# Optimization experiments

Measured on AMD Instinct MI355X. Metric: run time of the kernel, lower is better.

The kernel has to match this reference:

```python
import jax, jax.numpy as jnp
import numpy as np
from jax import lax

SPAN = 11
K = 2 * SPAN + 1          # 23 -> 529 offsets
SIG_RGB = 0.1
SIG_XY = 6.0
LAM = 0.15
B, C, H, W = 2, 3, 160, 160


def _patches(x):
    """x: (N, C, H, W) -> (N, C, K, K, H, W), zero-padded.
    patch[di, dj] at pixel (i, j) equals x[i + di - SPAN, j + dj - SPAN],
    matching the torch module's shifted-slice double loop (dx = di - SPAN)."""
    n, c, h, w = x.shape
    xp = jnp.pad(x, ((0, 0), (0, 0), (SPAN, SPAN), (SPAN, SPAN)))

    def get(off):
        di = off // K
        dj = off % K
        return lax.dynamic_slice(xp, (0, 0, di, dj), (n, c, h, w))

    p = jax.vmap(get)(jnp.arange(K * K))              # (K*K, N, C, H, W)
    return p.reshape(K, K, n, c, h, w).transpose(2, 3, 0, 1, 4, 5)


def setup_inputs() -> dict:
    key = jax.random.key(0)
    k1, k2, k3, k4, k5 = jax.random.split(key, 5)
    logit = jax.random.normal(k1, (B, C, H, W), jnp.float32)
    target = jax.random.randint(k2, (B, H, W), 0, C)
    # small-magnitude image so exp(-0.5*(x - patch/0.1)^2) does not fully underflow
    image = jax.random.uniform(k3, (B, 3, H, W), jnp.float32) * 0.1
    source_map = (jax.random.uniform(k4, (B, 1, H, W)) > 0.5).astype(jnp.float32)
    destination_map = (jax.random.uniform(k5, (B, H, W)) > 0.5).astype(jnp.float32)
    return dict(logit=logit, target=target, image=image,
                source_map=source_map, destination_map=destination_map)


def _gcrf(image, y_hat, source_map, m_dst):
    b, c, h, w = y_hat.shape
    img_p = _patches(image)                                  # (B,3,K,K,H,W)
    valid = _patches(jnp.ones((1, 1, h, w), image.dtype))[0, 0]  # (K,K,H,W) in-bounds mask
    # NOTE: faithful to source bug: only the shifted feature is divided by sigma
    drgb = image[:, :, None, None] - img_p / SIG_RGB
    k_rgb = jnp.exp(-0.5 * jnp.sum(drgb * drgb, axis=1))     # (B,K,K,H,W)
    ii, jj = jnp.meshgrid(jnp.arange(h, dtype=image.dtype),
                          jnp.arange(w, dtype=image.dtype), indexing='ij')
    idx = jnp.stack([ii, jj])[None]                          # (1,2,H,W)
    idx_p = _patches(idx)[0]                                 # (2,K,K,H,W)
    dxy = idx[0][:, None, None] - idx_p / SIG_XY
    k_xy = jnp.exp(-0.5 * jnp.sum(dxy * dxy, axis=0))        # (K,K,H,W)
    kmat = (k_rgb + k_xy[None]) * valid[None]                # out-of-bounds offsets stay 0
    m_src = _patches(source_map)[:, 0]                       # (B,K,K,H,W)
    Kg = kmat * m_src * m_dst[:, None, None]                 # gated kernel
    U = _patches(y_hat)                                      # (B,C,K,K,H,W)
    Egy = jnp.einsum('bcijhw,bijhw->bchw', U, Kg)            # sum over window
    temp = jnp.einsum('bchw,bdhw->bcd', Egy, y_hat)          # (B,C,C)
    Moff = 1.0 - jnp.eye(c, dtype=y_hat.dtype)               # off-diagonal compatibility
    return jnp.sum(Moff * temp) / (b * h * w)


def reference(logit, target, image, source_map, destination_map):
    y_hat = jax.nn.softmax(logit, axis=1)
    m_dst = 1.0 - destination_map
    L_gcrf = _gcrf(image, y_hat, source_map, m_dst)
    logp = jax.nn.log_softmax(logit, axis=1)
    L_ce = -jnp.take_along_axis(logp, target[:, None], axis=1)[:, 0]  # (B,H,W)
    L_ce = jnp.mean(L_ce * destination_map)
    return L_ce + LAM * L_gcrf
```

## Files before the change

kernel.cpp:

```cpp
#include <hip/hip_runtime.h>

#define Bn 2
#define Cn 3
#define Hn 160
#define Wn 160
#define SPANc 11
#define Kc 23
#define HWn (Hn * Wn)
#define PW 182
#define PP (PW * PW)
#define LAMc 0.15f
#define INVN (1.0f / (float)(Bn * HWn))
#define TJ 32
#define Gc 4
#define TI 32
#define NROW (TI + Kc - 1)
#define NREC (NROW * TJ)
#define CEXP (-0.72134752f)
#define CX   (14.42695041f)
#define CA   (0.72134752f)
#define NPREP ((Bn * PP + 255) / 256)

__device__ __forceinline__ float wave_reduce64(float v) {
#pragma unroll
    for (int off = 32; off > 0; off >>= 1) v += __shfl_down(v, off, 64);
    return v;
}

__device__ __forceinline__ unsigned int bf16pk(float a, float b) {
    unsigned int ua = __float_as_uint(a), ub = __float_as_uint(b);
    ua += 0x7fffu + ((ua >> 16) & 1u);
    ub += 0x7fffu + ((ub >> 16) & 1u);
    return (ua & 0xffff0000u) | (ub >> 16);
}

__global__ __launch_bounds__(256) void prep_kernel(
    const float* __restrict__ logit, const int* __restrict__ target,
    const float* __restrict__ image, const float* __restrict__ srcmap,
    const float* __restrict__ dstmap, uint4* __restrict__ gU4,
    float4* __restrict__ cvec, float* __restrict__ pc, float* __restrict__ out)
{
    int idx = blockIdx.x * 256 + threadIdx.x;
    float ce = 0.0f;
    if (idx < Bn * PP) {
        int b   = idx / PP;
        int rem = idx - b * PP;
        int ip  = rem / PW;
        int jp  = rem - ip * PW;
        int i = ip - SPANc, j = jp - SPANc;
        if ((unsigned)i < (unsigned)Hn && (unsigned)j < (unsigned)Wn) {
            int r = i * Wn + j;
            int p = b * HWn + r;
            const float* lg = logit + (size_t)b * Cn * HWn + r;
            float l0 = lg[0], l1 = lg[HWn], l2 = lg[2 * HWn];
            float m = fmaxf(l0, fmaxf(l1, l2));
            float e0 = __expf(l0 - m), e1 = __expf(l1 - m), e2 = __expf(l2 - m);
            float s = e0 + e1 + e2;
            float inv = 1.0f / s;
            float y0 = e0 * inv, y1 = e1 * inv, y2 = e2 * inv;
            float lse = m + __logf(s);

            const float* im = image + (size_t)b * 3 * HWn + r;
            float p0 = im[0], p1 = im[HWn], p2 = im[2 * HWn];
            float sv = srcmap[p];
            float dv = dstmap[p];

            float B = (p0 * p0 + p1 * p1 + p2 * p2) * (100.0f * CA);
            gU4[idx] = make_uint4(bf16pk(p0, p1), bf16pk(p2, -B),
                                  bf16pk(sv * y0, sv * y1), bf16pk(sv * y2, 0.0f));

            float md = LAMc * (1.0f - dv) * INVN;
            cvec[p] = make_float4(md * (1.0f - y0), md * (1.0f - y1),
                                  md * (1.0f - y2), 0.0f);

            int t = target[p];
            float lt = (t == 0) ? l0 : ((t == 1) ? l1 : l2);
            ce = (lse - lt) * dv * INVN;
        } else {
            gU4[idx] = make_uint4(0u, 0u, 0u, 0u);
        }
    }
    if (idx == 0) out[0] = 0.0f;

    float v = wave_reduce64(ce);
    __shared__ float wsum[4];
    int tid = threadIdx.x;
    if ((tid & 63) == 0) wsum[tid >> 6] = v;
    __syncthreads();
    if (tid == 0) pc[blockIdx.x] = wsum[0] + wsum[1] + wsum[2] + wsum[3];
}

template<bool XY>
__device__ __forceinline__ void tap(float p0, float p1, float p2, float mB,
                                    float q0, float q1, float q2,
                                    float c0s, float c1s, float c2s, float mA,
                                    bool xy_on, float dy2, float dxv,
                                    float& e0, float& e1, float& e2)
{
    float e = fmaf(c0s, p0, fmaf(c1s, p1, fmaf(c2s, p2, mB)));
    float k = exp2f(e + mA);
    if constexpr (XY) {
        if (xy_on) k += exp2f(fmaf(dxv, dxv, dy2) * CEXP);
    }
    e0 = fmaf(k, q0, e0);
    e1 = fmaf(k, q1, e1);
    e2 = fmaf(k, q2, e2);
}

template<bool XY>
__device__ __forceinline__ void window_loop(
    const uint4* sU4, int lbase,
    const float* c0s, const float* c1s, const float* c2s, const float* mA,
    bool xy_on, float dy2, float fi0, float eg[Gc][3])
{
#pragma unroll
    for (int r = 0; r < 3; ++r) {
        uint4 ru = sU4[lbase + r * TJ];
        float p0 = __uint_as_float(ru.x & 0xffff0000u);
        float p1 = __uint_as_float(ru.x << 16);
        float p2 = __uint_as_float(ru.y & 0xffff0000u);
        float mB = __uint_as_float(ru.y << 16);
        float q0 = __uint_as_float(ru.z & 0xffff0000u);
        float q1 = __uint_as_float(ru.z << 16);
        float q2 = __uint_as_float(ru.w & 0xffff0000u);
        float dxb = XY ? (fi0 - (fi0 + (float)(r - SPANc)) * (1.0f / 6.0f)) : 0.0f;
#pragma unroll
        for (int c = 0; c < 3; ++c) {
            if (c > r) continue;
            tap<XY>(p0, p1, p2, mB, q0, q1, q2, c0s[c], c1s[c], c2s[c], mA[c],
                    xy_on, dy2, dxb + (float)c, eg[c][0], eg[c][1], eg[c][2]);
        }
    }
#pragma unroll 2
    for (int r = 3; r <= 22; ++r) {
        uint4 ru = sU4[lbase + r * TJ];
        float p0 = __uint_as_float(ru.x & 0xffff0000u);
        float p1 = __uint_as_float(ru.x << 16);
        float p2 = __uint_as_float(ru.y & 0xffff0000u);
        float mB = __uint_as_float(ru.y << 16);
        float q0 = __uint_as_float(ru.z & 0xffff0000u);
        float q1 = __uint_as_float(ru.z << 16);
        float q2 = __uint_as_float(ru.w & 0xffff0000u);
        float dxb = XY ? (fi0 - (fi0 + (float)(r - SPANc)) * (1.0f / 6.0f)) : 0.0f;
#pragma unroll
        for (int c = 0; c < Gc; ++c) {
            tap<XY>(p0, p1, p2, mB, q0, q1, q2, c0s[c], c1s[c], c2s[c], mA[c],
                    xy_on, dy2, dxb + (float)c, eg[c][0], eg[c][1], eg[c][2]);
        }
    }
#pragma unroll
    for (int r = 23; r <= 25; ++r) {
        uint4 ru = sU4[lbase + r * TJ];
        float p0 = __uint_as_float(ru.x & 0xffff0000u);
        float p1 = __uint_as_float(ru.x << 16);
        float p2 = __uint_as_float(ru.y & 0xffff0000u);
        float mB = __uint_as_float(ru.y << 16);
        float q0 = __uint_as_float(ru.z & 0xffff0000u);
        float q1 = __uint_as_float(ru.z << 16);
        float q2 = __uint_as_float(ru.w & 0xffff0000u);
        float dxb = XY ? (fi0 - (fi0 + (float)(r - SPANc)) * (1.0f / 6.0f)) : 0.0f;
#pragma unroll
        for (int c = 1; c < Gc; ++c) {
            if (c < r - 22) continue;
            tap<XY>(p0, p1, p2, mB, q0, q1, q2, c0s[c], c1s[c], c2s[c], mA[c],
                    xy_on, dy2, dxb + (float)c, eg[c][0], eg[c][1], eg[c][2]);
        }
    }
}

__global__ __launch_bounds__(256, 4) void gcrf_kernel(
    const uint4* __restrict__ gU4, const float4* __restrict__ cvec,
    const float* __restrict__ pc, float* __restrict__ out)
{
    __shared__ uint4 sU4[NREC];

    int tx = threadIdx.x;
    int ty = threadIdx.y;
    int tid = ty * TJ + tx;
    int jx = blockIdx.x;
    int j  = jx * TJ + tx;
    int by = blockIdx.y;
    int b  = by / 5;
    int it = by - b * 5;
    int i0g = it * TI + ty * Gc;
    int dj = blockIdx.z;

    size_t g0 = (size_t)b * PP + (size_t)(it * TI) * PW + (jx * TJ + dj);
    for (int n = tid; n < NREC; n += 256) {
        int rr = n >> 5, cc = n & 31;
        sU4[n] = gU4[g0 + (size_t)rr * PW + cc];
    }
    __syncthreads();

    int lbase = ty * Gc * TJ + tx;
    float c0s[Gc], c1s[Gc], c2s[Gc], mA[Gc];
#pragma unroll
    for (int c = 0; c < Gc; ++c) {
        uint4 cu = sU4[lbase + (c + SPANc) * TJ];
        float cc0 = __uint_as_float(cu.x & 0xffff0000u);
        float cc1 = __uint_as_float(cu.x << 16);
        float cc2 = __uint_as_float(cu.y & 0xffff0000u);
        c0s[c] = cc0 * CX; c1s[c] = cc1 * CX; c2s[c] = cc2 * CX;
        mA[c] = -CA * fmaf(cc0, cc0, fmaf(cc1, cc1, cc2 * cc2));
    }

    bool xy_on = (j < 16) && (i0g < 16);
    float dy = (float)j - (float)(j + dj - SPANc) * (1.0f / 6.0f);
    float dy2 = dy * dy;
    float fi0 = (float)i0g;

    float eg[Gc][3];
#pragma unroll
    for (int c = 0; c < Gc; ++c) { eg[c][0] = 0.f; eg[c][1] = 0.f; eg[c][2] = 0.f; }

    if (jx == 0 && it == 0) {
        window_loop<true>(sU4, lbase, c0s, c1s, c2s, mA, xy_on, dy2, fi0, eg);
    } else {
        window_loop<false>(sU4, lbase, c0s, c1s, c2s, mA, false, dy2, fi0, eg);
    }

    const float4* cv = cvec + ((size_t)b * HWn + (size_t)i0g * Wn + j);
    float contrib = 0.0f;
#pragma unroll
    for (int c = 0; c < Gc; ++c) {
        float4 t = cv[(size_t)c * Wn];
        contrib += eg[c][0] * t.x + eg[c][1] * t.y + eg[c][2] * t.z;
    }

    float v = wave_reduce64(contrib);
    __shared__ float wsum[4];
    if ((tid & 63) == 0) wsum[tid >> 6] = v;
    __syncthreads();
    if (tid == 0) atomicAdd(out, wsum[0] + wsum[1] + wsum[2] + wsum[3]);

    if (jx == 4 && by == 9 && dj == 22) {
        float s = 0.0f;
        if (tid < NPREP) s += pc[tid];
        if (tid + 256 < NPREP) s += pc[tid + 256];
        float v2 = wave_reduce64(s);
        __syncthreads();
        if ((tid & 63) == 0) wsum[tid >> 6] = v2;
        __syncthreads();
        if (tid == 0) atomicAdd(out, wsum[0] + wsum[1] + wsum[2] + wsum[3]);
    }
}

extern "C" void kernel_launch(void* const* d_in, const int* in_sizes, int n_in,
                              void* d_out, int out_size, void* d_ws, size_t ws_size,
                              hipStream_t stream)
{
    const float* logit  = (const float*)d_in[0];
    const int*   target = (const int*)d_in[1];
    const float* image  = (const float*)d_in[2];
    const float* srcmap = (const float*)d_in[3];
    const float* dstmap = (const float*)d_in[4];
    float* out = (float*)d_out;

    const size_t NRECG = (size_t)Bn * PP;
    float*  pc   = (float*)((char*)d_ws + 256);
    uint4*  gU4  = (uint4*)((char*)d_ws + 4096);
    float4* cvec = (float4*)((char*)d_ws + 4096 + NRECG * 16);

    prep_kernel<<<NPREP, 256, 0, stream>>>(logit, target, image, srcmap, dstmap,
                                           gU4, cvec, pc, out);
    dim3 grid(Wn / TJ, (Hn / TI) * Bn, Kc);
    dim3 blk(TJ, 8);
    gcrf_kernel<<<grid, blk, 0, stream>>>(gU4, cvec, pc, out);
}
```

Measured before the change: 86.14 us.

## Split vertical window across two grid halves to increase block parallelism

Each block now processes either the upper (offsets -11..0) or lower (+1..+11) half of the vertical window, doubling the grid along z and shrinking the shared-memory tile to 43 rows. Launch bounds target 6 blocks per CU instead of 4. This aims to improve occupancy and load balance across CUs, at the cost of more redundant halo loads from global memory and twice as many atomic adds.

After: 99.32 us. +15.3%, slower.

```diff
diff --git a/kernel.cpp b/kernel.cpp
--- a/kernel.cpp
+++ b/kernel.cpp
@@ -14,8 +14,8 @@
 #define TJ 32
 #define Gc 4
 #define TI 32
-#define NROW (TI + Kc - 1)
-#define NREC (NROW * TJ)
+#define NROW2 43
+#define NREC2 (NROW2 * TJ)
 #define CEXP (-0.72134752f)
 #define CX   (14.42695041f)
 #define CA   (0.72134752f)
@@ -90,6 +90,17 @@
     if (tid == 0) pc[blockIdx.x] = wsum[0] + wsum[1] + wsum[2] + wsum[3];
 }
 
+__device__ __forceinline__ void unpk(uint4 ru, float& p0, float& p1, float& p2,
+                                     float& mB, float& q0, float& q1, float& q2) {
+    p0 = __uint_as_float(ru.x & 0xffff0000u);
+    p1 = __uint_as_float(ru.x << 16);
+    p2 = __uint_as_float(ru.y & 0xffff0000u);
+    mB = __uint_as_float(ru.y << 16);
+    q0 = __uint_as_float(ru.z & 0xffff0000u);
+    q1 = __uint_as_float(ru.z << 16);
+    q2 = __uint_as_float(ru.w & 0xffff0000u);
+}
+
 template<bool XY>
 __device__ __forceinline__ void tap(float p0, float p1, float p2, float mB,
                                     float q0, float q1, float q2,
@@ -107,41 +118,31 @@
     e2 = fmaf(k, q2, e2);
 }
 
-template<bool XY>
-__device__ __forceinline__ void window_loop(
+template<bool XY, int DH>
+__device__ __forceinline__ void window_loop2(
     const uint4* sU4, int lbase,
     const float* c0s, const float* c1s, const float* c2s, const float* mA,
     bool xy_on, float dy2, float fi0, float eg[Gc][3])
 {
 #pragma unroll
-    for (int r = 0; r < 3; ++r) {
+    for (int r = DH; r < 4; ++r) {
         uint4 ru = sU4[lbase + r * TJ];
-        float p0 = __uint_as_float(ru.x & 0xffff0000u);
-        float p1 = __uint_as_float(ru.x << 16);
-        float p2 = __uint_as_float(ru.y & 0xffff0000u);
-        float mB = __uint_as_float(ru.y << 16);
-        float q0 = __uint_as_float(ru.z & 0xffff0000u);
-        float q1 = __uint_as_float(ru.z << 16);
-        float q2 = __uint_as_float(ru.w & 0xffff0000u);
-        float dxb = XY ? (fi0 - (fi0 + (float)(r - SPANc)) * (1.0f / 6.0f)) : 0.0f;
-#pragma unroll
-        for (int c = 0; c < 3; ++c) {
-            if (c > r) continue;
+        float p0, p1, p2, mB, q0, q1, q2;
+        unpk(ru, p0, p1, p2, mB, q0, q1, q2);
+        float dxb = XY ? (fi0 - (fi0 + (float)(r - (DH ? 0 : SPANc))) * (1.0f / 6.0f)) : 0.0f;
+#pragma unroll
+        for (int c = 0; c < Gc; ++c) {
+            if (c > r - DH) continue;
             tap<XY>(p0, p1, p2, mB, q0, q1, q2, c0s[c], c1s[c], c2s[c], mA[c],
                     xy_on, dy2, dxb + (float)c, eg[c][0], eg[c][1], eg[c][2]);
         }
     }
 #pragma unroll 2
-    for (int r = 3; r <= 22; ++r) {
+    for (int r = 4; r <= 11; ++r) {
         uint4 ru = sU4[lbase + r * TJ];
-        float p0 = __uint_as_float(ru.x & 0xffff0000u);
-        float p1 = __uint_as_float(ru.x << 16);
-        float p2 = __uint_as_float(ru.y & 0xffff0000u);
-        float mB = __uint_as_float(ru.y << 16);
-        float q0 = __uint_as_float(ru.z & 0xffff0000u);
-        float q1 = __uint_as_float(ru.z << 16);
-        float q2 = __uint_as_float(ru.w & 0xffff0000u);
-        float dxb = XY ? (fi0 - (fi0 + (float)(r - SPANc)) * (1.0f / 6.0f)) : 0.0f;
+        float p0, p1, p2, mB, q0, q1, q2;
+        unpk(ru, p0, p1, p2, mB, q0, q1, q2);
+        float dxb = XY ? (fi0 - (fi0 + (float)(r - (DH ? 0 : SPANc))) * (1.0f / 6.0f)) : 0.0f;
 #pragma unroll
         for (int c = 0; c < Gc; ++c) {
             tap<XY>(p0, p1, p2, mB, q0, q1, q2, c0s[c], c1s[c], c2s[c], mA[c],
@@ -149,30 +150,25 @@
         }
     }
 #pragma unroll
-    for (int r = 23; r <= 25; ++r) {
+    for (int r = 12; r <= 14; ++r) {
         uint4 ru = sU4[lbase + r * TJ];
-        float p0 = __uint_as_float(ru.x & 0xffff0000u);
-        float p1 = __uint_as_float(ru.x << 16);
-        float p2 = __uint_as_float(ru.y & 0xffff0000u);
-        float mB = __uint_as_float(ru.y << 16);
-        float q0 = __uint_as_float(ru.z & 0xffff0000u);
-        float q1 = __uint_as_float(ru.z << 16);
-        float q2 = __uint_as_float(ru.w & 0xffff0000u);
-        float dxb = XY ? (fi0 - (fi0 + (float)(r - SPANc)) * (1.0f / 6.0f)) : 0.0f;
-#pragma unroll
-        for (int c = 1; c < Gc; ++c) {
-            if (c < r - 22) continue;
+        float p0, p1, p2, mB, q0, q1, q2;
+        unpk(ru, p0, p1, p2, mB, q0, q1, q2);
+        float dxb = XY ? (fi0 - (fi0 + (float)(r - (DH ? 0 : SPANc))) * (1.0f / 6.0f)) : 0.0f;
+#pragma unroll
+        for (int c = 0; c < Gc; ++c) {
+            if (c < r - SPANc) continue;
             tap<XY>(p0, p1, p2, mB, q0, q1, q2, c0s[c], c1s[c], c2s[c], mA[c],
                     xy_on, dy2, dxb + (float)c, eg[c][0], eg[c][1], eg[c][2]);
         }
     }
 }
 
-__global__ __launch_bounds__(256, 4) void gcrf_kernel(
+__global__ __launch_bounds__(256, 6) void gcrf_kernel(
     const uint4* __restrict__ gU4, const float4* __restrict__ cvec,
     const float* __restrict__ pc, float* __restrict__ out)
 {
-    __shared__ uint4 sU4[NREC];
+    __shared__ uint4 sU4[NREC2];
 
     int tx = threadIdx.x;
     int ty = threadIdx.y;
@@ -183,20 +179,24 @@
     int b  = by / 5;
     int it = by - b * 5;
     int i0g = it * TI + ty * Gc;
-    int dj = blockIdx.z;
-
-    size_t g0 = (size_t)b * PP + (size_t)(it * TI) * PW + (jx * TJ + dj);
-    for (int n = tid; n < NREC; n += 256) {
+    int zz = blockIdx.z;
+    int dh = (zz >= Kc) ? 1 : 0;
+    int dj = zz - dh * Kc;
+    int rbase = dh ? SPANc : 0;
+
+    size_t g0 = (size_t)b * PP + (size_t)(it * TI + rbase) * PW + (jx * TJ + dj);
+    for (int n = tid; n < NREC2; n += 256) {
         int rr = n >> 5, cc = n & 31;
         sU4[n] = gU4[g0 + (size_t)rr * PW + cc];
     }
     __syncthreads();
 
     int lbase = ty * Gc * TJ + tx;
+    int crow = dh ? 0 : SPANc;
     float c0s[Gc], c1s[Gc], c2s[Gc], mA[Gc];
 #pragma unroll
     for (int c = 0; c < Gc; ++c) {
-        uint4 cu = sU4[lbase + (c + SPANc) * TJ];
+        uint4 cu = sU4[lbase + (c + crow) * TJ];
         float cc0 = __uint_as_float(cu.x & 0xffff0000u);
         float cc1 = __uint_as_float(cu.x << 16);
         float cc2 = __uint_as_float(cu.y & 0xffff0000u);
@@ -214,9 +214,11 @@
     for (int c = 0; c < Gc; ++c) { eg[c][0] = 0.f; eg[c][1] = 0.f; eg[c][2] = 0.f; }
 
     if (jx == 0 && it == 0) {
-        window_loop<true>(sU4, lbase, c0s, c1s, c2s, mA, xy_on, dy2, fi0, eg);
+        if (dh) window_loop2<true, 1>(sU4, lbase, c0s, c1s, c2s, mA, xy_on, dy2, fi0, eg);
+        else    window_loop2<true, 0>(sU4, lbase, c0s, c1s, c2s, mA, xy_on, dy2, fi0, eg);
     } else {
-        window_loop<false>(sU4, lbase, c0s, c1s, c2s, mA, false, dy2, fi0, eg);
+        if (dh) window_loop2<false, 1>(sU4, lbase, c0s, c1s, c2s, mA, false, dy2, fi0, eg);
+        else    window_loop2<false, 0>(sU4, lbase, c0s, c1s, c2s, mA, false, dy2, fi0, eg);
     }
 
     const float4* cv = cvec + ((size_t)b * HWn + (size_t)i0g * Wn + j);
@@ -233,7 +235,7 @@
     __syncthreads();
     if (tid == 0) atomicAdd(out, wsum[0] + wsum[1] + wsum[2] + wsum[3]);
 
-    if (jx == 4 && by == 9 && dj == 22) {
+    if (jx == 4 && by == 9 && zz == 45) {
         float s = 0.0f;
         if (tid < NPREP) s += pc[tid];
         if (tid + 256 < NPREP) s += pc[tid + 256];
@@ -263,7 +265,7 @@
 
     prep_kernel<<<NPREP, 256, 0, stream>>>(logit, target, image, srcmap, dstmap,
                                            gU4, cvec, pc, out);
-    dim3 grid(Wn / TJ, (Hn / TI) * Bn, Kc);
+    dim3 grid(Wn / TJ, (Hn / TI) * Bn, 2 * Kc);
     dim3 blk(TJ, 8);
     gcrf_kernel<<<grid, blk, 0, stream>>>(gU4, cvec, pc, out);
 }
```
